# Kernel optimization log

Measured on AMD Instinct MI355X. Metric: run time of the kernel, lower is better.

Reference implementation:

```python
import jax, jax.numpy as jnp
import numpy as np

B, T, D_MODEL, HEAD_DIM = 16, 4096, 512, 64


def setup_inputs() -> dict:
    key = jax.random.key(0)
    kx, kq, kk, kv = jax.random.split(key, 4)
    x = jax.random.normal(kx, (B, T, D_MODEL), dtype=jnp.float32)
    # torch nn.Linear weights, stored pre-transposed as [in, out] for x @ W
    s = 1.0 / np.sqrt(D_MODEL)
    Wq = jax.random.uniform(kq, (D_MODEL, HEAD_DIM), jnp.float32, -s, s)
    Wk = jax.random.uniform(kk, (D_MODEL, HEAD_DIM), jnp.float32, -s, s)
    Wv = jax.random.uniform(kv, (D_MODEL, HEAD_DIM), jnp.float32, -s, s)
    return {"x": x, "Wq": Wq, "Wk": Wk, "Wv": Wv}


def reference(x, Wq, Wk, Wv):
    # Single-head causal self-attention (dropout in eval mode = identity)
    q = x @ Wq  # [B, T, h]
    k = x @ Wk
    v = x @ Wv
    scale = 1.0 / np.sqrt(HEAD_DIM).astype(np.float32)
    scores = jnp.einsum("bth,bsh->bts", q, k) * scale  # [B, T, T]
    t = scores.shape[1]
    causal = jnp.tril(jnp.ones((t, t), dtype=bool))
    scores = jnp.where(causal, scores, -jnp.inf)
    weights = jax.nn.softmax(scores, axis=-1)
    return jnp.einsum("bts,bsh->bth", weights, v)  # [B, T, h]
```

## Files before the change

kernel.cpp:

```cpp
#include <hip/hip_runtime.h>
#include <hip/hip_bf16.h>
#include <math.h>


#define NB 16
#define NT 4096
#define DMODEL 512
#define HD 64
#define CEXP 0.18033688011112042f

typedef unsigned short u16;
typedef unsigned int u32;
typedef __attribute__((ext_vector_type(2))) unsigned int u32x2;
typedef __attribute__((ext_vector_type(8))) short bf16x8;
typedef __attribute__((ext_vector_type(4))) float f32x4;
typedef __attribute__((ext_vector_type(16))) float f32x16;

__device__ __forceinline__ u16 bfu(float x) {
  __hip_bfloat16 h = __float2bfloat16(x);
  return *(u16*)&h;
}

__device__ __forceinline__ u32 cvtpk(float lo, float hi) {
  u32 r;
  asm("v_cvt_pk_bf16_f32 %0, %1, %2" : "=v"(r) : "v"(lo), "v"(hi));
  return r;
}

__device__ __forceinline__ u32x2 lane_swap(u32 a, u32 b) {
  asm("v_permlane32_swap_b32 %0, %1" : "+v"(a), "+v"(b));
  u32x2 r; r[0] = a; r[1] = b; return r;
}

__device__ __forceinline__ void gload16(const void* g, void* l) {
  __builtin_amdgcn_global_load_lds(
      (const __attribute__((address_space(1))) void*)g,
      (__attribute__((address_space(3))) void*)l, 16, 0, 0);
}

#define MFMA32(a, b, c) __builtin_amdgcn_mfma_f32_16x16x32_bf16(a, b, c, 0, 0, 0)
#define WMFMA(a, b, c)  __builtin_amdgcn_mfma_f32_32x32x16_bf16(a, b, c, 0, 0, 0)
#define LD8(p) (*(const bf16x8*)(p))

__global__ void prep_wt(const float* __restrict__ Wq, const float* __restrict__ Wk,
                        const float* __restrict__ Wv, u16* __restrict__ Wt) {
  int k0 = blockIdx.x * 16;
  int t = threadIdx.x;
#pragma unroll
  for (int i = 0; i < 12; ++i) {
    int idx = t + i * 256;
    int n = idx % 192;
    int kk = idx / 192;
    const float* W = (n < 64) ? Wq : (n < 128) ? Wk : Wv;
    float w = W[(size_t)(k0 + kk) * 64 + (n & 63)];
    Wt[(size_t)n * 512 + k0 + kk] = bfu(w);
  }
}

__global__ __launch_bounds__(512) void proj_qkv(const float* __restrict__ x,
                                                const u16* __restrict__ Wt,
                                                u16* __restrict__ qo,
                                                u16* __restrict__ ko,
                                                u16* __restrict__ vo) {
  __shared__ u16 As[128][48];
  int t = threadIdx.x;
  int m0 = blockIdx.x * 128;
  int lane = t & 63, wid = t >> 6;
  int wr = wid >> 2, wc = wid & 3;
  int g = lane >> 4, li = lane & 15;
  f32x4 acc[4][3];
#pragma unroll
  for (int i = 0; i < 4; ++i)
#pragma unroll
    for (int j = 0; j < 3; ++j) acc[i][j] = (f32x4){0.f, 0.f, 0.f, 0.f};

  int row = t >> 2, quad = t & 3;
  const float* srcb = x + (size_t)(m0 + row) * DMODEL + quad * 8;

  float4 pa0[2], pa1[2];
  pa0[0] = *(const float4*)(srcb);       pa1[0] = *(const float4*)(srcb + 4);
  pa0[1] = *(const float4*)(srcb + 32);  pa1[1] = *(const float4*)(srcb + 36);

#pragma unroll
  for (int s = 0; s < 16; ++s) {
    float4 c0 = pa0[s & 1], c1 = pa1[s & 1];
    if (s + 2 < 16) {
      pa0[s & 1] = *(const float4*)(srcb + (s + 2) * 32);
      pa1[s & 1] = *(const float4*)(srcb + (s + 2) * 32 + 4);
    }
    __syncthreads();
    union { u16 u[8]; bf16x8 v; } tmp;
    tmp.u[0] = bfu(c0.x); tmp.u[1] = bfu(c0.y);
    tmp.u[2] = bfu(c0.z); tmp.u[3] = bfu(c0.w);
    tmp.u[4] = bfu(c1.x); tmp.u[5] = bfu(c1.y);
    tmp.u[6] = bfu(c1.z); tmp.u[7] = bfu(c1.w);
    *(bf16x8*)&As[row][quad * 8] = tmp.v;
    __syncthreads();

    int k0 = s * 32;
    bf16x8 a[4], bb[3];
#pragma unroll
    for (int mf = 0; mf < 4; ++mf)
      a[mf] = *(const bf16x8*)&As[wr * 64 + mf * 16 + li][g * 8];
#pragma unroll
    for (int nf = 0; nf < 3; ++nf)
      bb[nf] = *(const bf16x8*)(Wt + (size_t)(wc * 48 + nf * 16 + li) * 512 + k0 + g * 8);
#pragma unroll
    for (int mf = 0; mf < 4; ++mf)
#pragma unroll
      for (int nf = 0; nf < 3; ++nf)
        acc[mf][nf] = MFMA32(a[mf], bb[nf], acc[mf][nf]);
  }

#pragma unroll
  for (int nf = 0; nf < 3; ++nf) {
    int n = wc * 48 + nf * 16 + li;
    if (n < 64) {
      int col = n;
#pragma unroll
      for (int mf = 0; mf < 4; ++mf)
#pragma unroll
        for (int r = 0; r < 4; ++r) {
          int m = m0 + wr * 64 + mf * 16 + 4 * g + r;
          qo[(size_t)m * HD + col] = bfu(acc[mf][nf][r] * CEXP);
        }
    } else if (n < 128) {
      int col = n & 63;
      int dt = col >> 4, hh = (col >> 3) & 1, jj = col & 7;
      size_t fo = (size_t)(dt * 2 + hh) * 256 + jj;
#pragma unroll
      for (int mf = 0; mf < 4; ++mf)
#pragma unroll
        for (int r = 0; r < 4; ++r) {
          int m = m0 + wr * 64 + mf * 16 + 4 * g + r;
          ko[(size_t)(m >> 5) * 2048 + fo + (m & 31) * 8] = bfu(acc[mf][nf][r]);
        }
    } else {
      int d = n - 128;
      int dh = d >> 5, l31d = d & 31;
#pragma unroll
      for (int mf = 0; mf < 4; ++mf) {
        int mbase = m0 + wr * 64 + mf * 16 + 4 * g;
        int kk2 = mbase & 31;
        int kt2 = kk2 >> 4, hh = (kk2 >> 3) & 1;
        size_t off = (size_t)(mbase >> 5) * 2048 +
                     (size_t)((dh * 2 + kt2) * 2 + hh) * 256 + l31d * 8 + (mbase & 7);
        ushort4 pk;
        pk.x = bfu(acc[mf][nf][0]);
        pk.y = bfu(acc[mf][nf][1]);
        pk.z = bfu(acc[mf][nf][2]);
        pk.w = bfu(acc[mf][nf][3]);
        *(ushort4*)(vo + off) = pk;
      }
    }
  }
}

__global__ __launch_bounds__(256, 2) void attn_fwd11(const u16* __restrict__ qg,
                                                     const u16* __restrict__ kg,
                                                     const u16* __restrict__ vg,
                                                     float* __restrict__ out) {
  __shared__ __align__(16) char smem[65536];
  u16* KV = (u16*)smem;
  float* MrgF = (float*)smem;

  int tid = threadIdx.x;
  int lane = tid & 63, w = tid >> 6;
  int l31 = lane & 31, h = lane >> 5;
  int qi = w >> 1, ki = w & 1;

  int f = blockIdx.x;
  int xcd = f & 7, i = f >> 3;
  int b = 2 * xcd + (i & 1);
  int bp = 63 - (i >> 1);

  const int limb = 2 * bp + 1;
  const int diagw = 2 * bp + qi;
  const int nr = (bp + 2) >> 1;
  const int q0w = bp * 64 + qi * 32;

  const u16* qb = qg + (size_t)b * NT * HD;
  const u16* kbs = kg + (size_t)b * NT * HD;
  const u16* vbs = vg + (size_t)b * NT * HD;
  float* ob = out + (size_t)b * NT * HD;

  bf16x8 qf[4];
#pragma unroll
  for (int dt = 0; dt < 4; ++dt)
    qf[dt] = LD8(qb + (size_t)(q0w + l31) * HD + dt * 16 + 8 * h);

  f32x16 oacc0, oacc1;
#pragma unroll
  for (int r = 0; r < 16; ++r) { oacc0[r] = 0.f; oacc1[r] = 0.f; }
  float lsum = 0.f;

  auto STAGE = [&](u16* lb, int tg) {
    const u16* gk = kbs + (size_t)tg * 2048 + lane * 8;
    const u16* gv = vbs + (size_t)tg * 2048 + lane * 8;
    u16* dk = lb + w * 4096 + lane * 8;
#pragma unroll
    for (int ii = 0; ii < 4; ++ii) {
      gload16(gk + ii * 512, dk + ii * 512);
      gload16(gv + ii * 512, dk + 2048 + ii * 512);
    }
  };

  auto COMPUTE = [&](const u16* kp0, const u16* vp0, bool maskdiag) {
    bf16x8 kf[4], vf[4];
#pragma unroll
    for (int dt = 0; dt < 4; ++dt)
      kf[dt] = LD8(kp0 + dt * 512 + h * 256 + l31 * 8);
#pragma unroll
    for (int dv = 0; dv < 4; ++dv)
      vf[dv] = LD8(vp0 + dv * 512 + h * 256 + l31 * 8);

    f32x16 sv;
#pragma unroll
    for (int r = 0; r < 16; ++r) sv[r] = 0.f;
    sv = WMFMA(kf[0], qf[0], sv);
    sv = WMFMA(kf[1], qf[1], sv);
    sv = WMFMA(kf[2], qf[2], sv);
    sv = WMFMA(kf[3], qf[3], sv);

    if (maskdiag) {
#pragma unroll
      for (int r = 0; r < 16; ++r) {
        int key = (r & 3) + 8 * (r >> 2) + 4 * h;
        if (key > l31) sv[r] = -1e30f;
      }
    }

    float p[16];
#pragma unroll
    for (int r = 0; r < 16; ++r) p[r] = __builtin_amdgcn_exp2f(sv[r]);
    lsum += (((p[0] + p[1]) + (p[2] + p[3])) + ((p[4] + p[5]) + (p[6] + p[7]))) +
            (((p[8] + p[9]) + (p[10] + p[11])) + ((p[12] + p[13]) + (p[14] + p[15])));
    u32 A0 = cvtpk(p[0], p[1]),   A1 = cvtpk(p[2], p[3]);
    u32 B0 = cvtpk(p[4], p[5]),   B1 = cvtpk(p[6], p[7]);
    u32 C0 = cvtpk(p[8], p[9]),   C1 = cvtpk(p[10], p[11]);
    u32 E0 = cvtpk(p[12], p[13]), E1 = cvtpk(p[14], p[15]);
    u32x2 s0 = lane_swap(A0, B0), s1 = lane_swap(A1, B1);
    u32x2 s2 = lane_swap(C0, E0), s3 = lane_swap(C1, E1);
    union { u32 d[4]; bf16x8 v; } f0u, f1u;
    f0u.d[0] = s0[0]; f0u.d[1] = s1[0]; f0u.d[2] = s0[1]; f0u.d[3] = s1[1];
    f1u.d[0] = s2[0]; f1u.d[1] = s3[0]; f1u.d[2] = s2[1]; f1u.d[3] = s3[1];

    oacc0 = WMFMA(vf[0], f0u.v, oacc0);
    oacc1 = WMFMA(vf[2], f0u.v, oacc1);
    oacc0 = WMFMA(vf[1], f1u.v, oacc0);
    oacc1 = WMFMA(vf[3], f1u.v, oacc1);
  };

  STAGE(KV, min(w, limb));

  int cur = 0;
  for (int jr = 0; jr < nr; ++jr) {
    if (jr + 1 < nr) {
      STAGE(KV + (cur ^ 1) * 16384, min(4 * (jr + 1) + w, limb));
      asm volatile("s_waitcnt vmcnt(8)" ::: "memory");
    } else {
      asm volatile("s_waitcnt vmcnt(0)" ::: "memory");
    }
    __builtin_amdgcn_sched_barrier(0);
    asm volatile("s_barrier" ::: "memory");

    const u16* kv0 = KV + cur * 16384;
    int j1 = 4 * jr + ki, j2 = 4 * jr + 2 + ki;
    __builtin_amdgcn_s_setprio(1);
    if (j1 <= diagw)
      COMPUTE(kv0 + ki * 4096, kv0 + ki * 4096 + 2048, j1 == diagw);
    if (j2 <= diagw)
      COMPUTE(kv0 + (2 + ki) * 4096, kv0 + (2 + ki) * 4096 + 2048, j2 == diagw);
    __builtin_amdgcn_s_setprio(0);

    asm volatile("s_barrier" ::: "memory");
    cur ^= 1;
  }

  lsum += __shfl_xor(lsum, 32);
  {
    float* mg = MrgF + ((size_t)w * 64 + lane) * 33;
#pragma unroll
    for (int r = 0; r < 16; ++r) { mg[r] = oacc0[r]; mg[16 + r] = oacc1[r]; }
    mg[32] = lsum;
  }
  __syncthreads();
#pragma unroll
  for (int s = 0; s < 4; ++s) {
    int ql = (lane >> 2) + 16 * (s & 1);
    int dq = ki * 8 + (lane & 3) + 4 * (s >> 1);
    const float* m0p = MrgF + ((size_t)(qi * 2) * 64) * 33;
    const float* m1p = MrgF + ((size_t)(qi * 2 + 1) * 64) * 33;
    float ls = m0p[(size_t)ql * 33 + 32] + m1p[(size_t)ql * 33 + 32];
    float inv = 1.0f / ls;
    f32x4 o4;
#pragma unroll
    for (int dd = 0; dd < 4; ++dd) {
      int d = dq * 4 + dd;
      int dh = d >> 5, rem = d & 31;
      int srch = (rem >> 2) & 1;
      int reg = dh * 16 + (rem & 3) + ((rem >> 3) << 2);
      size_t ro = (size_t)(ql + 32 * srch) * 33 + reg;
      o4[dd] = (m0p[ro] + m1p[ro]) * inv;
    }
    *(f32x4*)(ob + (size_t)(q0w + ql) * HD + dq * 4) = o4;
  }
}

extern "C" void kernel_launch(void* const* d_in, const int* in_sizes, int n_in,
                              void* d_out, int out_size, void* d_ws, size_t ws_size,
                              hipStream_t stream) {
  const float* x  = (const float*)d_in[0];
  const float* Wq = (const float*)d_in[1];
  const float* Wk = (const float*)d_in[2];
  const float* Wv = (const float*)d_in[3];
  float* out = (float*)d_out;

  u16* Wt  = (u16*)d_ws;
  u16* qws = (u16*)((char*)d_ws + 192 * 512 * 2);
  u16* kws = qws + (size_t)NB * NT * HD;
  u16* vws = kws + (size_t)NB * NT * HD;

  prep_wt<<<32, 256, 0, stream>>>(Wq, Wk, Wv, Wt);
  proj_qkv<<<(NB * NT) / 128, 512, 0, stream>>>(x, Wt, qws, kws, vws);
  attn_fwd11<<<1024, 256, 0, stream>>>(qws, kws, vws, out);
}
```

Measured before the change: 91.39 us.

## Double query rows per block to reuse staged K/V tiles across two query subtiles

```diff
diff --git a/kernel.cpp b/kernel.cpp
--- a/kernel.cpp
+++ b/kernel.cpp
@@ -156,7 +156,7 @@
   }
 }
 
-__global__ __launch_bounds__(256, 2) void attn_fwd11(const u16* __restrict__ qg,
+__global__ __launch_bounds__(256, 2) void attn_fwd12(const u16* __restrict__ qg,
                                                      const u16* __restrict__ kg,
                                                      const u16* __restrict__ vg,
                                                      float* __restrict__ out) {
@@ -167,32 +167,36 @@
   int tid = threadIdx.x;
   int lane = tid & 63, w = tid >> 6;
   int l31 = lane & 31, h = lane >> 5;
-  int qi = w >> 1, ki = w & 1;
+  int qi2 = w >> 1, ki = w & 1;
 
   int f = blockIdx.x;
   int xcd = f & 7, i = f >> 3;
-  int b = 2 * xcd + (i & 1);
-  int bp = 63 - (i >> 1);
-
-  const int limb = 2 * bp + 1;
-  const int diagw = 2 * bp + qi;
-  const int nr = (bp + 2) >> 1;
-  const int q0w = bp * 64 + qi * 32;
+  int b, bp;
+  if (i < 32) { b = 2 * xcd;     bp = 31 - i; }
+  else        { b = 2 * xcd + 1; bp = i - 32; }
+
+  const int limb = 4 * bp + 3;
+  const int d0 = 4 * bp + 2 * qi2;
+  const int d1 = d0 + 1;
+  const int nr = bp + 1;
+  const int q0w = bp * 128 + qi2 * 64;
 
   const u16* qb = qg + (size_t)b * NT * HD;
   const u16* kbs = kg + (size_t)b * NT * HD;
   const u16* vbs = vg + (size_t)b * NT * HD;
   float* ob = out + (size_t)b * NT * HD;
 
-  bf16x8 qf[4];
-#pragma unroll
-  for (int dt = 0; dt < 4; ++dt)
-    qf[dt] = LD8(qb + (size_t)(q0w + l31) * HD + dt * 16 + 8 * h);
-
-  f32x16 oacc0, oacc1;
-#pragma unroll
-  for (int r = 0; r < 16; ++r) { oacc0[r] = 0.f; oacc1[r] = 0.f; }
-  float lsum = 0.f;
+  bf16x8 qf0[4], qf1[4];
+#pragma unroll
+  for (int dt = 0; dt < 4; ++dt) {
+    qf0[dt] = LD8(qb + (size_t)(q0w + l31) * HD + dt * 16 + 8 * h);
+    qf1[dt] = LD8(qb + (size_t)(q0w + 32 + l31) * HD + dt * 16 + 8 * h);
+  }
+
+  f32x16 oa00, oa01, oa10, oa11;
+#pragma unroll
+  for (int r = 0; r < 16; ++r) { oa00[r] = 0.f; oa01[r] = 0.f; oa10[r] = 0.f; oa11[r] = 0.f; }
+  float lsum0 = 0.f, lsum1 = 0.f;
 
   auto STAGE = [&](u16* lb, int tg) {
     const u16* gk = kbs + (size_t)tg * 2048 + lane * 8;
@@ -205,22 +209,15 @@
     }
   };
 
-  auto COMPUTE = [&](const u16* kp0, const u16* vp0, bool maskdiag) {
-    bf16x8 kf[4], vf[4];
-#pragma unroll
-    for (int dt = 0; dt < 4; ++dt)
-      kf[dt] = LD8(kp0 + dt * 512 + h * 256 + l31 * 8);
-#pragma unroll
-    for (int dv = 0; dv < 4; ++dv)
-      vf[dv] = LD8(vp0 + dv * 512 + h * 256 + l31 * 8);
-
+  auto SUB = [&](const bf16x8 (&qfs)[4], const bf16x8 (&kf)[4], const bf16x8 (&vf)[4],
+                 f32x16& oA, f32x16& oB, float& ls, bool maskdiag) {
     f32x16 sv;
 #pragma unroll
     for (int r = 0; r < 16; ++r) sv[r] = 0.f;
-    sv = WMFMA(kf[0], qf[0], sv);
-    sv = WMFMA(kf[1], qf[1], sv);
-    sv = WMFMA(kf[2], qf[2], sv);
-    sv = WMFMA(kf[3], qf[3], sv);
+    sv = WMFMA(kf[0], qfs[0], sv);
+    sv = WMFMA(kf[1], qfs[1], sv);
+    sv = WMFMA(kf[2], qfs[2], sv);
+    sv = WMFMA(kf[3], qfs[3], sv);
 
     if (maskdiag) {
 #pragma unroll
@@ -233,8 +230,8 @@
     float p[16];
 #pragma unroll
     for (int r = 0; r < 16; ++r) p[r] = __builtin_amdgcn_exp2f(sv[r]);
-    lsum += (((p[0] + p[1]) + (p[2] + p[3])) + ((p[4] + p[5]) + (p[6] + p[7]))) +
-            (((p[8] + p[9]) + (p[10] + p[11])) + ((p[12] + p[13]) + (p[14] + p[15])));
+    ls += (((p[0] + p[1]) + (p[2] + p[3])) + ((p[4] + p[5]) + (p[6] + p[7]))) +
+          (((p[8] + p[9]) + (p[10] + p[11])) + ((p[12] + p[13]) + (p[14] + p[15])));
     u32 A0 = cvtpk(p[0], p[1]),   A1 = cvtpk(p[2], p[3]);
     u32 B0 = cvtpk(p[4], p[5]),   B1 = cvtpk(p[6], p[7]);
     u32 C0 = cvtpk(p[8], p[9]),   C1 = cvtpk(p[10], p[11]);
@@ -245,10 +242,22 @@
     f0u.d[0] = s0[0]; f0u.d[1] = s1[0]; f0u.d[2] = s0[1]; f0u.d[3] = s1[1];
     f1u.d[0] = s2[0]; f1u.d[1] = s3[0]; f1u.d[2] = s2[1]; f1u.d[3] = s3[1];
 
-    oacc0 = WMFMA(vf[0], f0u.v, oacc0);
-    oacc1 = WMFMA(vf[2], f0u.v, oacc1);
-    oacc0 = WMFMA(vf[1], f1u.v, oacc0);
-    oacc1 = WMFMA(vf[3], f1u.v, oacc1);
+    oA = WMFMA(vf[0], f0u.v, oA);
+    oB = WMFMA(vf[2], f0u.v, oB);
+    oA = WMFMA(vf[1], f1u.v, oA);
+    oB = WMFMA(vf[3], f1u.v, oB);
+  };
+
+  auto COMPUTE = [&](const u16* kp0, const u16* vp0, int j) {
+    bf16x8 kf[4], vf[4];
+#pragma unroll
+    for (int dt = 0; dt < 4; ++dt)
+      kf[dt] = LD8(kp0 + dt * 512 + h * 256 + l31 * 8);
+#pragma unroll
+    for (int dv = 0; dv < 4; ++dv)
+      vf[dv] = LD8(vp0 + dv * 512 + h * 256 + l31 * 8);
+    if (j <= d0) SUB(qf0, kf, vf, oa00, oa01, lsum0, j == d0);
+    if (j <= d1) SUB(qf1, kf, vf, oa10, oa11, lsum1, j == d1);
   };
 
   STAGE(KV, min(w, limb));
@@ -267,43 +276,48 @@
     const u16* kv0 = KV + cur * 16384;
     int j1 = 4 * jr + ki, j2 = 4 * jr + 2 + ki;
     __builtin_amdgcn_s_setprio(1);
-    if (j1 <= diagw)
-      COMPUTE(kv0 + ki * 4096, kv0 + ki * 4096 + 2048, j1 == diagw);
-    if (j2 <= diagw)
-      COMPUTE(kv0 + (2 + ki) * 4096, kv0 + (2 + ki) * 4096 + 2048, j2 == diagw);
+    if (j1 <= d1) COMPUTE(kv0 + ki * 4096, kv0 + ki * 4096 + 2048, j1);
+    if (j2 <= d1) COMPUTE(kv0 + (2 + ki) * 4096, kv0 + (2 + ki) * 4096 + 2048, j2);
     __builtin_amdgcn_s_setprio(0);
 
     asm volatile("s_barrier" ::: "memory");
     cur ^= 1;
   }
 
-  lsum += __shfl_xor(lsum, 32);
-  {
-    float* mg = MrgF + ((size_t)w * 64 + lane) * 33;
-#pragma unroll
-    for (int r = 0; r < 16; ++r) { mg[r] = oacc0[r]; mg[16 + r] = oacc1[r]; }
-    mg[32] = lsum;
-  }
-  __syncthreads();
-#pragma unroll
-  for (int s = 0; s < 4; ++s) {
-    int ql = (lane >> 2) + 16 * (s & 1);
-    int dq = ki * 8 + (lane & 3) + 4 * (s >> 1);
-    const float* m0p = MrgF + ((size_t)(qi * 2) * 64) * 33;
-    const float* m1p = MrgF + ((size_t)(qi * 2 + 1) * 64) * 33;
-    float ls = m0p[(size_t)ql * 33 + 32] + m1p[(size_t)ql * 33 + 32];
-    float inv = 1.0f / ls;
-    f32x4 o4;
-#pragma unroll
-    for (int dd = 0; dd < 4; ++dd) {
-      int d = dq * 4 + dd;
-      int dh = d >> 5, rem = d & 31;
-      int srch = (rem >> 2) & 1;
-      int reg = dh * 16 + (rem & 3) + ((rem >> 3) << 2);
-      size_t ro = (size_t)(ql + 32 * srch) * 33 + reg;
-      o4[dd] = (m0p[ro] + m1p[ro]) * inv;
-    }
-    *(f32x4*)(ob + (size_t)(q0w + ql) * HD + dq * 4) = o4;
+  float ls0 = lsum0 + __shfl_xor(lsum0, 32);
+  float ls1 = lsum1 + __shfl_xor(lsum1, 32);
+#pragma unroll
+  for (int s = 0; s < 2; ++s) {
+    __syncthreads();
+    {
+      float* mg = MrgF + ((size_t)w * 64 + lane) * 33;
+      const f32x16& oA = s ? oa10 : oa00;
+      const f32x16& oB = s ? oa11 : oa01;
+#pragma unroll
+      for (int r = 0; r < 16; ++r) { mg[r] = oA[r]; mg[16 + r] = oB[r]; }
+      mg[32] = s ? ls1 : ls0;
+    }
+    __syncthreads();
+    const float* m0p = MrgF + ((size_t)(qi2 * 2) * 64) * 33;
+    const float* m1p = MrgF + ((size_t)(qi2 * 2 + 1) * 64) * 33;
+#pragma unroll
+    for (int t2 = 0; t2 < 4; ++t2) {
+      int ql = (lane >> 2) + 16 * (t2 & 1);
+      int dq = ki * 8 + (lane & 3) + 4 * (t2 >> 1);
+      float ls = m0p[(size_t)ql * 33 + 32] + m1p[(size_t)ql * 33 + 32];
+      float inv = 1.0f / ls;
+      f32x4 o4;
+#pragma unroll
+      for (int dd = 0; dd < 4; ++dd) {
+        int d = dq * 4 + dd;
+        int dh = d >> 5, rem = d & 31;
+        int srch = (rem >> 2) & 1;
+        int reg = dh * 16 + (rem & 3) + ((rem >> 3) << 2);
+        size_t ro = (size_t)(ql + 32 * srch) * 33 + reg;
+        o4[dd] = (m0p[ro] + m1p[ro]) * inv;
+      }
+      *(f32x4*)(ob + (size_t)(q0w + s * 32 + ql) * HD + dq * 4) = o4;
+    }
   }
 }
 
@@ -323,5 +337,5 @@
 
   prep_wt<<<32, 256, 0, stream>>>(Wq, Wk, Wv, Wt);
   proj_qkv<<<(NB * NT) / 128, 512, 0, stream>>>(x, Wt, qws, kws, vws);
-  attn_fwd11<<<1024, 256, 0, stream>>>(qws, kws, vws, out);
-}
+  attn_fwd12<<<512, 256, 0, stream>>>(qws, kws, vws, out);
+}
```

After: 92.88 us. Within noise of the previous version (+1.6%).

## Restructure QKV projection so each wave owns 16 rows, dropping LDS staging

Applied to the files above, without the earlier changes.

```diff
diff --git a/kernel.cpp b/kernel.cpp
--- a/kernel.cpp
+++ b/kernel.cpp
@@ -57,106 +57,87 @@
   }
 }
 
-__global__ __launch_bounds__(512) void proj_qkv(const float* __restrict__ x,
-                                                const u16* __restrict__ Wt,
-                                                u16* __restrict__ qo,
-                                                u16* __restrict__ ko,
-                                                u16* __restrict__ vo) {
-  __shared__ u16 As[128][48];
+__global__ __launch_bounds__(512, 4) void proj_qkv(const float* __restrict__ x,
+                                                   const u16* __restrict__ Wt,
+                                                   u16* __restrict__ qo,
+                                                   u16* __restrict__ ko,
+                                                   u16* __restrict__ vo) {
   int t = threadIdx.x;
   int m0 = blockIdx.x * 128;
-  int lane = t & 63, wid = t >> 6;
-  int wr = wid >> 2, wc = wid & 3;
+  int lane = t & 63, w = t >> 6;
   int g = lane >> 4, li = lane & 15;
-  f32x4 acc[4][3];
-#pragma unroll
-  for (int i = 0; i < 4; ++i)
-#pragma unroll
-    for (int j = 0; j < 3; ++j) acc[i][j] = (f32x4){0.f, 0.f, 0.f, 0.f};
-
-  int row = t >> 2, quad = t & 3;
-  const float* srcb = x + (size_t)(m0 + row) * DMODEL + quad * 8;
-
-  float4 pa0[2], pa1[2];
-  pa0[0] = *(const float4*)(srcb);       pa1[0] = *(const float4*)(srcb + 4);
-  pa0[1] = *(const float4*)(srcb + 32);  pa1[1] = *(const float4*)(srcb + 36);
+
+  f32x4 acc[12];
+#pragma unroll
+  for (int nf = 0; nf < 12; ++nf) acc[nf] = (f32x4){0.f, 0.f, 0.f, 0.f};
+
+  const float* xb = x + (size_t)(m0 + w * 16 + li) * DMODEL + g * 8;
+  const u16* wb = Wt + (size_t)li * 512 + g * 8;
+
+  float4 pa[2], pb[2];
+#pragma unroll
+  for (int s = 0; s < 2; ++s) {
+    pa[s] = *(const float4*)(xb + s * 32);
+    pb[s] = *(const float4*)(xb + s * 32 + 4);
+  }
 
 #pragma unroll
   for (int s = 0; s < 16; ++s) {
-    float4 c0 = pa0[s & 1], c1 = pa1[s & 1];
+    float4 c0 = pa[s & 1], c1 = pb[s & 1];
     if (s + 2 < 16) {
-      pa0[s & 1] = *(const float4*)(srcb + (s + 2) * 32);
-      pa1[s & 1] = *(const float4*)(srcb + (s + 2) * 32 + 4);
-    }
-    __syncthreads();
-    union { u16 u[8]; bf16x8 v; } tmp;
-    tmp.u[0] = bfu(c0.x); tmp.u[1] = bfu(c0.y);
-    tmp.u[2] = bfu(c0.z); tmp.u[3] = bfu(c0.w);
-    tmp.u[4] = bfu(c1.x); tmp.u[5] = bfu(c1.y);
-    tmp.u[6] = bfu(c1.z); tmp.u[7] = bfu(c1.w);
-    *(bf16x8*)&As[row][quad * 8] = tmp.v;
-    __syncthreads();
-
-    int k0 = s * 32;
-    bf16x8 a[4], bb[3];
-#pragma unroll
-    for (int mf = 0; mf < 4; ++mf)
-      a[mf] = *(const bf16x8*)&As[wr * 64 + mf * 16 + li][g * 8];
-#pragma unroll
-    for (int nf = 0; nf < 3; ++nf)
-      bb[nf] = *(const bf16x8*)(Wt + (size_t)(wc * 48 + nf * 16 + li) * 512 + k0 + g * 8);
-#pragma unroll
-    for (int mf = 0; mf < 4; ++mf)
-#pragma unroll
-      for (int nf = 0; nf < 3; ++nf)
-        acc[mf][nf] = MFMA32(a[mf], bb[nf], acc[mf][nf]);
-  }
-
-#pragma unroll
-  for (int nf = 0; nf < 3; ++nf) {
-    int n = wc * 48 + nf * 16 + li;
+      pa[s & 1] = *(const float4*)(xb + (s + 2) * 32);
+      pb[s & 1] = *(const float4*)(xb + (s + 2) * 32 + 4);
+    }
+    union { u16 u[8]; bf16x8 v; } af;
+    af.u[0] = bfu(c0.x); af.u[1] = bfu(c0.y);
+    af.u[2] = bfu(c0.z); af.u[3] = bfu(c0.w);
+    af.u[4] = bfu(c1.x); af.u[5] = bfu(c1.y);
+    af.u[6] = bfu(c1.z); af.u[7] = bfu(c1.w);
+    const u16* wp = wb + s * 32;
+#pragma unroll
+    for (int nf = 0; nf < 12; ++nf) {
+      bf16x8 bfrag = LD8(wp + (size_t)nf * 16 * 512);
+      acc[nf] = MFMA32(af.v, bfrag, acc[nf]);
+    }
+  }
+
+#pragma unroll
+  for (int nf = 0; nf < 12; ++nf) {
+    int n = nf * 16 + li;
     if (n < 64) {
-      int col = n;
-#pragma unroll
-      for (int mf = 0; mf < 4; ++mf)
-#pragma unroll
-        for (int r = 0; r < 4; ++r) {
-          int m = m0 + wr * 64 + mf * 16 + 4 * g + r;
-          qo[(size_t)m * HD + col] = bfu(acc[mf][nf][r] * CEXP);
-        }
+#pragma unroll
+      for (int r = 0; r < 4; ++r) {
+        int m = m0 + w * 16 + 4 * g + r;
+        qo[(size_t)m * HD + n] = bfu(acc[nf][r] * CEXP);
+      }
     } else if (n < 128) {
       int col = n & 63;
       int dt = col >> 4, hh = (col >> 3) & 1, jj = col & 7;
       size_t fo = (size_t)(dt * 2 + hh) * 256 + jj;
 #pragma unroll
-      for (int mf = 0; mf < 4; ++mf)
-#pragma unroll
-        for (int r = 0; r < 4; ++r) {
-          int m = m0 + wr * 64 + mf * 16 + 4 * g + r;
-          ko[(size_t)(m >> 5) * 2048 + fo + (m & 31) * 8] = bfu(acc[mf][nf][r]);
-        }
+      for (int r = 0; r < 4; ++r) {
+        int m = m0 + w * 16 + 4 * g + r;
+        ko[(size_t)(m >> 5) * 2048 + fo + (m & 31) * 8] = bfu(acc[nf][r]);
+      }
     } else {
       int d = n - 128;
       int dh = d >> 5, l31d = d & 31;
-#pragma unroll
-      for (int mf = 0; mf < 4; ++mf) {
-        int mbase = m0 + wr * 64 + mf * 16 + 4 * g;
-        int kk2 = mbase & 31;
-        int kt2 = kk2 >> 4, hh = (kk2 >> 3) & 1;
-        size_t off = (size_t)(mbase >> 5) * 2048 +
-                     (size_t)((dh * 2 + kt2) * 2 + hh) * 256 + l31d * 8 + (mbase & 7);
-        ushort4 pk;
-        pk.x = bfu(acc[mf][nf][0]);
-        pk.y = bfu(acc[mf][nf][1]);
-        pk.z = bfu(acc[mf][nf][2]);
-        pk.w = bfu(acc[mf][nf][3]);
-        *(ushort4*)(vo + off) = pk;
-      }
-    }
-  }
-}
-
-__global__ __launch_bounds__(256, 2) void attn_fwd11(const u16* __restrict__ qg,
+      int mbase = m0 + w * 16 + 4 * g;
+      int kk2 = mbase & 31;
+      int kt2 = kk2 >> 4, hh = (kk2 >> 3) & 1;
+      size_t off = (size_t)(mbase >> 5) * 2048 +
+                   (size_t)((dh * 2 + kt2) * 2 + hh) * 256 + l31d * 8 + (mbase & 7);
+      ushort4 pk;
+      pk.x = bfu(acc[nf][0]);
+      pk.y = bfu(acc[nf][1]);
+      pk.z = bfu(acc[nf][2]);
+      pk.w = bfu(acc[nf][3]);
+      *(ushort4*)(vo + off) = pk;
+    }
+  }
+}
+
+__global__ __launch_bounds__(256, 2) void attn_fwd17(const u16* __restrict__ qg,
                                                      const u16* __restrict__ kg,
                                                      const u16* __restrict__ vg,
                                                      float* __restrict__ out) {
@@ -323,5 +304,5 @@
 
   prep_wt<<<32, 256, 0, stream>>>(Wq, Wk, Wv, Wt);
   proj_qkv<<<(NB * NT) / 128, 512, 0, stream>>>(x, Wt, qws, kws, vws);
-  attn_fwd11<<<1024, 256, 0, stream>>>(qws, kws, vws, out);
-}
+  attn_fwd17<<<1024, 256, 0, stream>>>(qws, kws, vws, out);
+}
```

After: 156.4 us. 1.71x slower.
